# Performance work log

Measured on AMD Instinct MI355X. Metric: run time of the kernel, lower is better.

## Reference

```python
import jax, jax.numpy as jnp
import numpy as np

B, H, W, C = 2, 256, 256, 96
HEADS, WS, K = 6, 16, 64
HID = C // 8          # MoE hidden (reduction=8)
MLP = 2 * C           # mlp_ratio=2
KS = 5                # convffn / lepe kernel
N = H * W
WSQ = WS * WS
HEAD_D = C // HEADS


def _dwconv(x, w, b, pad):
    # x: [B,C,H,W], w: [C,1,k,k] depthwise conv
    y = jax.lax.conv_general_dilated(x, w, (1, 1), [(pad, pad), (pad, pad)],
        dimension_numbers=('NCHW', 'OIHW', 'NCHW'), feature_group_count=x.shape[1])
    return y + b[None, :, None, None]


def _ln(x, g, b):
    mu = x.mean(-1, keepdims=True)
    var = ((x - mu) ** 2).mean(-1, keepdims=True)
    return (x - mu) * jax.lax.rsqrt(var + 1e-5) * g + b


def _gelu(x):
    return jax.nn.gelu(x, approximate=False)


def _lrelu(x):
    return jnp.where(x >= 0, x, 0.2 * x)


def _make_rpi():
    coords = np.stack(np.meshgrid(np.arange(WS), np.arange(WS), indexing='ij'))
    cf = coords.reshape(2, -1)
    rel = (cf[:, :, None] - cf[:, None, :]).transpose(1, 2, 0).astype(np.int32)
    rel[..., 0] += WS - 1
    rel[..., 1] += WS - 1
    rel[..., 0] *= 2 * WS - 1
    return jnp.asarray(rel.sum(-1))  # [WSQ, WSQ]


def setup_inputs():
    key = jax.random.key(0)
    ks = iter(jax.random.split(key, 64))
    nrm = lambda shape, s=0.02: jax.random.normal(next(ks), shape, jnp.float32) * s
    inp = {}
    inp['x'] = jax.random.normal(next(ks), (B, N, C), jnp.float32)
    inp['n1_g'] = jnp.ones((C,), jnp.float32); inp['n1_b'] = jnp.zeros((C,), jnp.float32)
    inp['n2_g'] = jnp.ones((C,), jnp.float32); inp['n2_b'] = jnp.zeros((C,), jnp.float32)
    inp['g_w1'] = nrm((HID, C)); inp['g_b1'] = jnp.zeros((HID,), jnp.float32)
    inp['g_w2'] = nrm((3, HID)); inp['g_b2'] = jnp.zeros((3,), jnp.float32)
    for i, k_sz in zip((1, 2, 3), (3, 5, 7)):
        inp[f'e{i}_w1'] = nrm((HID, C)); inp[f'e{i}_b1'] = jnp.zeros((HID,), jnp.float32)
        inp[f'e{i}_pw'] = nrm((HID, HID))
        inp[f'e{i}_dw'] = nrm((HID, 1, k_sz, k_sz), 0.1); inp[f'e{i}_dwb'] = jnp.zeros((HID,), jnp.float32)
        inp[f'e{i}_w2'] = nrm((C, HID)); inp[f'e{i}_b2'] = jnp.zeros((C,), jnp.float32)
    inp['moe_scale'] = jnp.full((1,), 0.001, jnp.float32)
    inp['qkv_w'] = nrm((3 * C, C)); inp['qkv_b'] = jnp.zeros((3 * C,), jnp.float32)
    inp['lepe_w'] = nrm((C, 1, KS, KS), 0.1); inp['lepe_b'] = jnp.zeros((C,), jnp.float32)
    inp['rpb'] = nrm(((2 * WS - 1) ** 2, HEADS))
    inp['proj_w'] = nrm((C, C)); inp['proj_b'] = jnp.zeros((C,), jnp.float32)
    inp['fc1_w'] = nrm((MLP, C)); inp['fc1_b'] = jnp.zeros((MLP,), jnp.float32)
    inp['ffn_dw'] = nrm((MLP, 1, KS, KS), 0.1); inp['ffn_db'] = jnp.zeros((MLP,), jnp.float32)
    inp['fc2_w'] = nrm((C, MLP)); inp['fc2_b'] = jnp.zeros((C,), jnp.float32)
    inp['rpi'] = _make_rpi()
    return inp


def _forward(x, n1_g, n1_b, n2_g, n2_b, g_w1, g_b1, g_w2, g_b2,
             e1_w1, e1_b1, e1_pw, e1_dw, e1_dwb, e1_w2, e1_b2,
             e2_w1, e2_b1, e2_pw, e2_dw, e2_dwb, e2_w2, e2_b2,
             e3_w1, e3_b1, e3_pw, e3_dw, e3_dwb, e3_w2, e3_b2,
             moe_scale, qkv_w, qkv_b, lepe_w, lepe_b, rpb, proj_w, proj_b,
             fc1_w, fc1_b, ffn_dw, ffn_db, fc2_w, fc2_b, rpi):
    b, n, c = x.shape
    shortcut = x
    y = _ln(x, n1_g, n1_b)
    img = y.reshape(b, H, W, c).transpose(0, 3, 1, 2)  # [b,c,H,W]

    # ---- MultiScaleMoEBlock ----
    pooled = img.mean((2, 3))                                   # [b,c]
    g = jax.nn.relu(pooled @ g_w1.T + g_b1)
    g = jax.nn.softmax(g @ g_w2.T + g_b2, axis=-1)              # [b,3]

    def expert(z, w1, b1, pw, dw, dwb, w2, b2, pad):
        t = _lrelu(jnp.einsum('bchw,oc->bohw', z, w1) + b1[None, :, None, None])
        t = jnp.einsum('bchw,oc->bohw', t, pw)                  # BSConvU pw (no bias)
        t = _lrelu(_dwconv(t, dw, dwb, pad))                    # BSConvU dw
        return jnp.einsum('bchw,oc->bohw', t, w2) + b2[None, :, None, None]

    o = (g[:, 0, None, None, None] * expert(img, e1_w1, e1_b1, e1_pw, e1_dw, e1_dwb, e1_w2, e1_b2, 1)
         + g[:, 1, None, None, None] * expert(img, e2_w1, e2_b1, e2_pw, e2_dw, e2_dwb, e2_w2, e2_b2, 2)
         + g[:, 2, None, None, None] * expert(img, e3_w1, e3_b1, e3_pw, e3_dw, e3_dwb, e3_w2, e3_b2, 3))
    img = img + o * moe_scale[0]
    y = img.transpose(0, 2, 3, 1).reshape(b, n, c)

    # ---- qkv + LePE ----
    qkv = y @ qkv_w.T + qkv_b                                   # [b,n,3c]
    v = qkv[..., 2 * c:]
    vimg = v.reshape(b, H, W, c).transpose(0, 3, 1, 2)
    lepe = _gelu(_dwconv(vimg, lepe_w, lepe_b, (KS - 1) // 2)).transpose(0, 2, 3, 1).reshape(b, n, c)
    xq = jnp.concatenate([qkv, lepe], -1).reshape(b, H, W, 4 * c)

    # ---- window partition (shift=0) ----
    win = xq.reshape(b, H // WS, WS, W // WS, WS, 4 * c).transpose(0, 1, 3, 2, 4, 5).reshape(-1, WSQ, 4 * c)
    Bw = win.shape[0]
    qkvl = win.reshape(Bw, WSQ, 4, HEADS, HEAD_D).transpose(2, 0, 3, 1, 4)
    q, k_, vv, lp = qkvl[0], qkvl[1], qkvl[2], qkvl[3]          # each [Bw,H,N,d]

    attn = jnp.einsum('bhnd,bhmd->bhnm', q * (HEAD_D ** -0.5), k_)
    bias = rpb[rpi].transpose(2, 0, 1)                          # [heads,WSQ,WSQ]
    attn = jax.nn.softmax(attn + bias[None], axis=-1)

    # top-k progressive focused attention (first layer: pfa is None)
    vals, idx = jax.lax.top_k(attn, K)                          # [Bw,heads,WSQ,K]
    bi = jnp.arange(Bw)[:, None, None, None]
    hi = jnp.arange(HEADS)[None, :, None, None]
    ni = jnp.arange(WSQ)[None, None, :, None]
    attn_s = jnp.zeros_like(attn).at[bi, hi, ni, idx].set(vals)
    out = jnp.einsum('bhnm,bhmd->bhnd', attn_s, vv) + lp
    out = out.transpose(0, 2, 1, 3).reshape(Bw, WSQ, c)
    out = out @ proj_w.T + proj_b

    # ---- window reverse ----
    out = out.reshape(b, H // WS, W // WS, WS, WS, c).transpose(0, 1, 3, 2, 4, 5).reshape(b, n, c)
    x = shortcut + out

    # ---- ConvFFN ----
    y = _ln(x, n2_g, n2_b)
    t = _gelu(y @ fc1_w.T + fc1_b)
    timg = t.reshape(b, H, W, MLP).transpose(0, 3, 1, 2)
    t = t + _gelu(_dwconv(timg, ffn_dw, ffn_db, (KS - 1) // 2)).transpose(0, 2, 3, 1).reshape(b, n, MLP)
    x = x + (t @ fc2_w.T + fc2_b)
    return x


def reference(x, n1_g, n1_b, n2_g, n2_b, g_w1, g_b1, g_w2, g_b2,
              e1_w1, e1_b1, e1_pw, e1_dw, e1_dwb, e1_w2, e1_b2,
              e2_w1, e2_b1, e2_pw, e2_dw, e2_dwb, e2_w2, e2_b2,
              e3_w1, e3_b1, e3_pw, e3_dw, e3_dwb, e3_w2, e3_b2,
              moe_scale, qkv_w, qkv_b, lepe_w, lepe_b, rpb, proj_w, proj_b,
              fc1_w, fc1_b, ffn_dw, ffn_db, fc2_w, fc2_b, rpi):
    return _forward(x, n1_g, n1_b, n2_g, n2_b, g_w1, g_b1, g_w2, g_b2,
                    e1_w1, e1_b1, e1_pw, e1_dw, e1_dwb, e1_w2, e1_b2,
                    e2_w1, e2_b1, e2_pw, e2_dw, e2_dwb, e2_w2, e2_b2,
                    e3_w1, e3_b1, e3_pw, e3_dw, e3_dwb, e3_w2, e3_b2,
                    moe_scale, qkv_w, qkv_b, lepe_w, lepe_b, rpb, proj_w, proj_b,
                    fc1_w, fc1_b, ffn_dw, ffn_db, fc2_w, fc2_b, rpi)
```

## Files before the change

### kernel.cpp

```cpp
#include <hip/hip_runtime.h>
#include <cstdint>

#define BB 2
#define HH_ 256
#define WW_ 256
#define CC 96
#define NTOK 65536
#define MTOK 131072
#define HEADS 6
#define WS 16
#define WSQ 256
#define HEAD_D 16
#define TOPK 64
#define HID 12
#define MLP_ 192

typedef short v8s __attribute__((ext_vector_type(8)));
typedef float v4f __attribute__((ext_vector_type(4)));

__device__ __forceinline__ float gelu_f(float v) {
  return 0.5f * v * (1.0f + erff(v * 0.70710678118654752440f));
}
__device__ __forceinline__ float lrelu_f(float v) { return v >= 0.0f ? v : 0.2f * v; }
__device__ __forceinline__ unsigned short bf16r(float f) {
  unsigned u = __float_as_uint(f);
  unsigned r = u + 0x7fffu + ((u >> 16) & 1u);
  return (unsigned short)(r >> 16);
}
__device__ __forceinline__ float bf16d(unsigned short h) {
  return __uint_as_float(((unsigned)h) << 16);
}

__global__ __launch_bounds__(256) void ln_kernel(const float* __restrict__ in,
    const float* __restrict__ gam, const float* __restrict__ bet, float* __restrict__ out) {
  int wid = blockIdx.x * 4 + (threadIdx.x >> 6);
  int lane = threadIdx.x & 63;
  const float* row = in + (size_t)wid * CC;
  float v0 = row[lane];
  float v1 = (lane < 32) ? row[64 + lane] : 0.0f;
  float s = v0 + v1;
  #pragma unroll
  for (int off = 32; off; off >>= 1) s += __shfl_xor(s, off);
  float mean = s * (1.0f / 96.0f);
  float d0 = v0 - mean;
  float d1 = (lane < 32) ? (v1 - mean) : 0.0f;
  float q = d0 * d0 + d1 * d1;
  #pragma unroll
  for (int off = 32; off; off >>= 1) q += __shfl_xor(q, off);
  float r = rsqrtf(q * (1.0f / 96.0f) + 1e-5f);
  float* orow = out + (size_t)wid * CC;
  orow[lane] = d0 * r * gam[lane] + bet[lane];
  if (lane < 32) orow[64 + lane] = d1 * r * gam[64 + lane] + bet[64 + lane];
}

__global__ __launch_bounds__(128) void pool_kernel(const float* __restrict__ A, float* __restrict__ pooled) {
  int c = threadIdx.x;
  if (c >= CC) return;
  int b = blockIdx.y;
  int t0 = blockIdx.x * 512;
  const float* base = A + ((size_t)b * NTOK + t0) * CC + c;
  float acc = 0.0f;
  #pragma unroll 8
  for (int t = 0; t < 512; t++) acc += base[(size_t)t * CC];
  atomicAdd(&pooled[b * CC + c], acc);
}

__global__ __launch_bounds__(64) void gate_kernel(const float* __restrict__ pooled,
    const float* __restrict__ w1, const float* __restrict__ b1,
    const float* __restrict__ w2, const float* __restrict__ b2, float* __restrict__ gv) {
  __shared__ float hb[BB][HID];
  __shared__ float lb[BB][3];
  int tid = threadIdx.x;
  if (tid < BB * HID) {
    int b = tid / HID, o = tid % HID;
    float s = b1[o];
    for (int c = 0; c < CC; c++) s += (pooled[b * CC + c] * (1.0f / 65536.0f)) * w1[o * CC + c];
    hb[b][o] = fmaxf(s, 0.0f);
  }
  __syncthreads();
  if (tid < BB * 3) {
    int b = tid / 3, j = tid % 3;
    float s = b2[j];
    for (int o = 0; o < HID; o++) s += hb[b][o] * w2[j * HID + o];
    lb[b][j] = s;
  }
  __syncthreads();
  if (tid < BB) {
    float m = fmaxf(lb[tid][0], fmaxf(lb[tid][1], lb[tid][2]));
    float e0 = __expf(lb[tid][0] - m), e1 = __expf(lb[tid][1] - m), e2 = __expf(lb[tid][2] - m);
    float inv = 1.0f / (e0 + e1 + e2);
    gv[tid * 3 + 0] = e0 * inv; gv[tid * 3 + 1] = e1 * inv; gv[tid * 3 + 2] = e2 * inv;
  }
}

template <int K, int NO, int ACT, bool RESID, bool HASB>
__global__ __launch_bounds__(256, 4) void mgemm_kernel(const float* __restrict__ A,
    const float* __restrict__ W, const float* __restrict__ bias,
    const float* __restrict__ resid, float* __restrict__ out, int ostride, int rstride) {
  __shared__ __align__(16) unsigned short al[128][104];
  __shared__ __align__(16) unsigned short wl[64][104];
  int tid = threadIdx.x;
  int lane = tid & 63, wv = tid >> 6, quad = lane >> 4, to = lane & 15;
  int o0 = blockIdx.x * 64, p0 = blockIdx.y * 128;
  v4f acc[2][4];
  #pragma unroll
  for (int ni = 0; ni < 4; ni++) {
    float bv = 0.0f;
    if (HASB) { int o = o0 + ni * 16 + to; if (o < NO) bv = bias[o]; }
    #pragma unroll
    for (int mi = 0; mi < 2; mi++) acc[mi][ni] = (v4f){bv, bv, bv, bv};
  }
  for (int kc = 0; kc < K; kc += 96) {
    __syncthreads();
    {
      int r = tid & 127, half = tid >> 7;
      const float* ap = A + (size_t)(p0 + r) * K + kc + half * 48;
      #pragma unroll
      for (int g = 0; g < 3; g++) {
        float4 f0 = *(const float4*)(ap + g * 16);
        float4 f1 = *(const float4*)(ap + g * 16 + 4);
        float4 f2 = *(const float4*)(ap + g * 16 + 8);
        float4 f3 = *(const float4*)(ap + g * 16 + 12);
        uint4 u, v;
        u.x = (unsigned)bf16r(f0.x) | ((unsigned)bf16r(f0.y) << 16);
        u.y = (unsigned)bf16r(f0.z) | ((unsigned)bf16r(f0.w) << 16);
        u.z = (unsigned)bf16r(f1.x) | ((unsigned)bf16r(f1.y) << 16);
        u.w = (unsigned)bf16r(f1.z) | ((unsigned)bf16r(f1.w) << 16);
        v.x = (unsigned)bf16r(f2.x) | ((unsigned)bf16r(f2.y) << 16);
        v.y = (unsigned)bf16r(f2.z) | ((unsigned)bf16r(f2.w) << 16);
        v.z = (unsigned)bf16r(f3.x) | ((unsigned)bf16r(f3.y) << 16);
        v.w = (unsigned)bf16r(f3.z) | ((unsigned)bf16r(f3.w) << 16);
        *(uint4*)&al[r][half * 48 + g * 16] = u;
        *(uint4*)&al[r][half * 48 + g * 16 + 8] = v;
      }
    }
    {
      int r = tid & 63, q = tid >> 6;
      int o = o0 + r;
      if (o < NO) {
        const float* wp = W + (size_t)o * K + kc + q * 24;
        #pragma unroll
        for (int g = 0; g < 3; g++) {
          float4 f0 = *(const float4*)(wp + g * 8);
          float4 f1 = *(const float4*)(wp + g * 8 + 4);
          uint4 u;
          u.x = (unsigned)bf16r(f0.x) | ((unsigned)bf16r(f0.y) << 16);
          u.y = (unsigned)bf16r(f0.z) | ((unsigned)bf16r(f0.w) << 16);
          u.z = (unsigned)bf16r(f1.x) | ((unsigned)bf16r(f1.y) << 16);
          u.w = (unsigned)bf16r(f1.z) | ((unsigned)bf16r(f1.w) << 16);
          *(uint4*)&wl[r][q * 24 + g * 8] = u;
        }
      } else {
        uint4 z = make_uint4(0, 0, 0, 0);
        #pragma unroll
        for (int g = 0; g < 3; g++) *(uint4*)&wl[r][q * 24 + g * 8] = z;
      }
    }
    __syncthreads();
    #pragma unroll
    for (int ks = 0; ks < 3; ks++) {
      v8s af[2], bfr[4];
      #pragma unroll
      for (int mi = 0; mi < 2; mi++)
        af[mi] = *(const v8s*)&al[wv * 32 + mi * 16 + to][ks * 32 + quad * 8];
      #pragma unroll
      for (int ni = 0; ni < 4; ni++)
        bfr[ni] = *(const v8s*)&wl[ni * 16 + to][ks * 32 + quad * 8];
      #pragma unroll
      for (int mi = 0; mi < 2; mi++)
        #pragma unroll
        for (int ni = 0; ni < 4; ni++)
          acc[mi][ni] = __builtin_amdgcn_mfma_f32_16x16x32_bf16(af[mi], bfr[ni], acc[mi][ni], 0, 0, 0);
    }
  }
  #pragma unroll
  for (int mi = 0; mi < 2; mi++)
    #pragma unroll
    for (int ni = 0; ni < 4; ni++) {
      int o = o0 + ni * 16 + to;
      if (o < NO) {
        #pragma unroll
        for (int rg = 0; rg < 4; rg++) {
          int p = p0 + wv * 32 + mi * 16 + quad * 4 + rg;
          float v = acc[mi][ni][rg];
          if (ACT == 1) v = lrelu_f(v);
          else if (ACT == 2) v = gelu_f(v);
          if (RESID) v += resid[(size_t)p * rstride + o];
          out[(size_t)p * ostride + o] = v;
        }
      }
    }
}

template <int K, int KC, int NO, int ACT, bool RESID, bool HASB>
__global__ __launch_bounds__(256) void gemm_kernel(const float* __restrict__ in,
    const float* __restrict__ w, const float* __restrict__ bias,
    const float* __restrict__ resid, float* __restrict__ out, int ostride, int rstride) {
  __shared__ __align__(16) float xs[64][KC + 4];
  __shared__ __align__(16) float ws[64][KC + 4];
  int tid = threadIdx.x;
  int p0 = blockIdx.x * 64;
  int o0 = blockIdx.y * 64;
  int to = tid & 15, tp = tid >> 4;
  float acc[4][4];
  #pragma unroll
  for (int j = 0; j < 4; j++) {
    float bv = 0.0f;
    if (HASB) { int o = o0 + to + 16 * j; if (o < NO) bv = bias[o]; }
    #pragma unroll
    for (int i = 0; i < 4; i++) acc[i][j] = bv;
  }
  for (int kc = 0; kc < K; kc += KC) {
    __syncthreads();
    for (int idx = tid; idx < 64 * (KC / 4); idx += 256) {
      int p = idx / (KC / 4), c4 = idx % (KC / 4);
      *(float4*)&xs[p][c4 * 4] = *(const float4*)&in[(size_t)(p0 + p) * K + kc + c4 * 4];
    }
    for (int idx = tid; idx < 64 * (KC / 4); idx += 256) {
      int r = idx / (KC / 4), c4 = idx % (KC / 4);
      int o = o0 + r;
      float4 v = make_float4(0.f, 0.f, 0.f, 0.f);
      if (o < NO) v = *(const float4*)&w[(size_t)o * K + kc + c4 * 4];
      *(float4*)&ws[r][c4 * 4] = v;
    }
    __syncthreads();
    #pragma unroll 4
    for (int cc = 0; cc < KC; cc += 4) {
      float4 xv[4], wv[4];
      #pragma unroll
      for (int i = 0; i < 4; i++) xv[i] = *(const float4*)&xs[tp + 16 * i][cc];
      #pragma unroll
      for (int j = 0; j < 4; j++) wv[j] = *(const float4*)&ws[to + 16 * j][cc];
      #pragma unroll
      for (int i = 0; i < 4; i++)
        #pragma unroll
        for (int j = 0; j < 4; j++)
          acc[i][j] += xv[i].x * wv[j].x + xv[i].y * wv[j].y + xv[i].z * wv[j].z + xv[i].w * wv[j].w;
    }
  }
  #pragma unroll
  for (int i = 0; i < 4; i++) {
    int p = p0 + tp + 16 * i;
    #pragma unroll
    for (int j = 0; j < 4; j++) {
      int o = o0 + to + 16 * j;
      if (o < NO) {
        float v = acc[i][j];
        if (ACT == 1) v = lrelu_f(v);
        else if (ACT == 2) v = gelu_f(v);
        if (RESID) v += resid[(size_t)p * rstride + o];
        out[(size_t)p * ostride + o] = v;
      }
    }
  }
}

template <int KSZ, int CH, int ACT, bool RESID>
__global__ __launch_bounds__(256) void dwconv_kernel(const float* __restrict__ in,
    const float* __restrict__ wt, const float* __restrict__ wb,
    const float* __restrict__ resid, float* __restrict__ out,
    int istride, int ostride, int rstride) {
  constexpr int C4 = CH / 4;
  constexpr int K2 = KSZ * KSZ;
  int e = blockIdx.x * 256 + threadIdx.x;
  int c4 = e % C4;
  int pix = e / C4;
  int b = pix >> 16, n = pix & 65535, h = n >> 8, w = n & 255;
  const int P = (KSZ - 1) / 2;
  int c = c4 * 4;
  float4 acc = *(const float4*)(wb + c);
  #pragma unroll
  for (int ky = 0; ky < KSZ; ky++) {
    int hh = h + ky - P;
    if (hh < 0 || hh >= HH_) continue;
    #pragma unroll
    for (int kx = 0; kx < KSZ; kx++) {
      int ww = w + kx - P;
      if (ww < 0 || ww >= WW_) continue;
      float4 iv = *(const float4*)(in + ((size_t)(b << 16) + (hh << 8) + ww) * istride + c);
      int t = ky * KSZ + kx;
      acc.x += wt[(c + 0) * K2 + t] * iv.x;
      acc.y += wt[(c + 1) * K2 + t] * iv.y;
      acc.z += wt[(c + 2) * K2 + t] * iv.z;
      acc.w += wt[(c + 3) * K2 + t] * iv.w;
    }
  }
  if (ACT == 1) {
    acc.x = lrelu_f(acc.x); acc.y = lrelu_f(acc.y); acc.z = lrelu_f(acc.z); acc.w = lrelu_f(acc.w);
  } else if (ACT == 2) {
    acc.x = gelu_f(acc.x); acc.y = gelu_f(acc.y); acc.z = gelu_f(acc.z); acc.w = gelu_f(acc.w);
  }
  if (RESID) {
    float4 rv = *(const float4*)(resid + (size_t)pix * rstride + c);
    acc.x += rv.x; acc.y += rv.y; acc.z += rv.z; acc.w += rv.w;
  }
  *(float4*)(out + (size_t)pix * ostride + c) = acc;
}

template <int KSZ, int CH, int ACT, bool RESID>
__global__ __launch_bounds__(256) void dwconv4_kernel(const float* __restrict__ in,
    const float* __restrict__ wt, const float* __restrict__ wb,
    const float* __restrict__ resid, float* __restrict__ out,
    int istride, int ostride, int rstride) {
  constexpr int C4 = CH / 4;
  constexpr int K2 = KSZ * KSZ;
  constexpr int P = (KSZ - 1) / 2;
  constexpr int NC = KSZ + 3;
  int e = blockIdx.x * 256 + threadIdx.x;
  int c4 = e % C4;
  int g = e / C4;
  int b = g >> 14, rem = g & 16383, h = rem >> 6, w0 = (rem & 63) << 2;
  int c = c4 * 4;
  float4 wbv = *(const float4*)(wb + c);
  float4 acc[4] = {wbv, wbv, wbv, wbv};
  #pragma unroll
  for (int ky = 0; ky < KSZ; ky++) {
    int hh = h + ky - P;
    if (hh < 0 || hh >= HH_) continue;
    const float* rowp = in + ((size_t)(b << 16) + (hh << 8)) * istride + c;
    float4 iv[NC];
    #pragma unroll
    for (int k = 0; k < NC; k++) {
      int ww = w0 - P + k;
      if (ww >= 0 && ww < WW_) iv[k] = *(const float4*)(rowp + (size_t)ww * istride);
      else iv[k] = make_float4(0.f, 0.f, 0.f, 0.f);
    }
    #pragma unroll
    for (int kx = 0; kx < KSZ; kx++) {
      int t = ky * KSZ + kx;
      float wt0 = wt[(c + 0) * K2 + t];
      float wt1 = wt[(c + 1) * K2 + t];
      float wt2 = wt[(c + 2) * K2 + t];
      float wt3 = wt[(c + 3) * K2 + t];
      #pragma unroll
      for (int px = 0; px < 4; px++) {
        acc[px].x += wt0 * iv[kx + px].x;
        acc[px].y += wt1 * iv[kx + px].y;
        acc[px].z += wt2 * iv[kx + px].z;
        acc[px].w += wt3 * iv[kx + px].w;
      }
    }
  }
  #pragma unroll
  for (int px = 0; px < 4; px++) {
    float4 a = acc[px];
    if (ACT == 1) {
      a.x = lrelu_f(a.x); a.y = lrelu_f(a.y); a.z = lrelu_f(a.z); a.w = lrelu_f(a.w);
    } else if (ACT == 2) {
      a.x = gelu_f(a.x); a.y = gelu_f(a.y); a.z = gelu_f(a.z); a.w = gelu_f(a.w);
    }
    size_t pix = (size_t)(b << 16) + (h << 8) + w0 + px;
    if (RESID) {
      float4 rv = *(const float4*)(resid + pix * rstride + c);
      a.x += rv.x; a.y += rv.y; a.z += rv.z; a.w += rv.w;
    }
    *(float4*)(out + pix * ostride + c) = a;
  }
}

__global__ __launch_bounds__(256) void moe_combine_kernel(float* __restrict__ A,
    const float* __restrict__ t3a, const float* __restrict__ t3b, const float* __restrict__ t3c,
    const float* __restrict__ w2a, const float* __restrict__ w2b, const float* __restrict__ w2c,
    const float* __restrict__ b2a, const float* __restrict__ b2b, const float* __restrict__ b2c,
    const float* __restrict__ gv, const float* __restrict__ ms) {
  int e4 = blockIdx.x * 256 + threadIdx.x;
  int c4 = e4 % (CC / 4), pix = e4 / (CC / 4), b = pix >> 16;
  int c = c4 * 4;
  float4 sa = *(const float4*)(b2a + c);
  float4 sb = *(const float4*)(b2b + c);
  float4 sc = *(const float4*)(b2c + c);
  #pragma unroll
  for (int h2 = 0; h2 < HID; h2++) {
    float ta = t3a[(size_t)pix * HID + h2];
    float tb = t3b[(size_t)pix * HID + h2];
    float tc = t3c[(size_t)pix * HID + h2];
    sa.x += ta * w2a[(c + 0) * HID + h2]; sa.y += ta * w2a[(c + 1) * HID + h2];
    sa.z += ta * w2a[(c + 2) * HID + h2]; sa.w += ta * w2a[(c + 3) * HID + h2];
    sb.x += tb * w2b[(c + 0) * HID + h2]; sb.y += tb * w2b[(c + 1) * HID + h2];
    sb.z += tb * w2b[(c + 2) * HID + h2]; sb.w += tb * w2b[(c + 3) * HID + h2];
    sc.x += tc * w2c[(c + 0) * HID + h2]; sc.y += tc * w2c[(c + 1) * HID + h2];
    sc.z += tc * w2c[(c + 2) * HID + h2]; sc.w += tc * w2c[(c + 3) * HID + h2];
  }
  float g0 = gv[b * 3 + 0], g1 = gv[b * 3 + 1], g2 = gv[b * 3 + 2], m0 = ms[0];
  float* ap = A + (size_t)pix * CC + c;
  float4 av = *(const float4*)ap;
  av.x += m0 * (g0 * sa.x + g1 * sb.x + g2 * sc.x);
  av.y += m0 * (g0 * sa.y + g1 * sb.y + g2 * sc.y);
  av.z += m0 * (g0 * sa.z + g1 * sb.z + g2 * sc.z);
  av.w += m0 * (g0 * sa.w + g1 * sb.w + g2 * sc.w);
  *(float4*)ap = av;
}

__global__ __launch_bounds__(256) void bias_kernel(const int* __restrict__ rpi,
    const float* __restrict__ rpb, float* __restrict__ biasT) {
  int idx = blockIdx.x * 256 + threadIdx.x;
  int h = idx >> 16, nm = idx & 65535;
  int n = nm >> 8, m = nm & 255;
  biasT[(h << 16) + ((n >> 2) << 10) + (m << 2) + (n & 3)] = rpb[rpi[nm] * HEADS + h];
}

__global__ __launch_bounds__(256, 3) void attn_kernel(const float* __restrict__ X,
    const float* __restrict__ biasT, float* __restrict__ O) {
  __shared__ __align__(16) unsigned short kb[256][16];
  __shared__ __align__(16) unsigned short vt[16][264];
  __shared__ __align__(16) unsigned short sS[4][16][264];
  int tid = threadIdx.x;
  int wi = blockIdx.x, hh = blockIdx.y;
  int b = wi >> 8, wrem = wi & 255, wy = wrem >> 4, wx = wrem & 15;
  int lane = tid & 63, wv_ = tid >> 6, quad = lane >> 4, to = lane & 15;

  {
    int m = tid;
    int nm = (((wy << 4) + (m >> 4)) << 8) | ((wx << 4) + (m & 15));
    size_t xb = ((size_t)(b << 16) + nm) * 288 + hh * 16;
    float kr[16], vr[16];
    *(float4*)&kr[0]  = *(const float4*)(X + xb + 96);
    *(float4*)&kr[4]  = *(const float4*)(X + xb + 100);
    *(float4*)&kr[8]  = *(const float4*)(X + xb + 104);
    *(float4*)&kr[12] = *(const float4*)(X + xb + 108);
    *(float4*)&vr[0]  = *(const float4*)(X + xb + 192);
    *(float4*)&vr[4]  = *(const float4*)(X + xb + 196);
    *(float4*)&vr[8]  = *(const float4*)(X + xb + 200);
    *(float4*)&vr[12] = *(const float4*)(X + xb + 204);
    unsigned u_[8];
    #pragma unroll
    for (int i = 0; i < 8; i++)
      u_[i] = (unsigned)bf16r(kr[2 * i]) | ((unsigned)bf16r(kr[2 * i + 1]) << 16);
    *(uint4*)&kb[m][0] = make_uint4(u_[0], u_[1], u_[2], u_[3]);
    *(uint4*)&kb[m][8] = make_uint4(u_[4], u_[5], u_[6], u_[7]);
    #pragma unroll
    for (int d = 0; d < 16; d++) vt[d][m] = bf16r(vr[d]);
  }

  auto load_q = [&](int ch) -> v8s {
    v8s af = {0, 0, 0, 0, 0, 0, 0, 0};
    if (quad < 2) {
      int nq = (((wy << 4) + ch) << 8) | ((wx << 4) + to);
      const float* qp = X + ((size_t)(b << 16) + nq) * 288 + hh * 16 + quad * 8;
      float4 f0 = *(const float4*)qp;
      float4 f1 = *(const float4*)(qp + 4);
      uint4 u;
      u.x = (unsigned)bf16r(f0.x * 0.25f) | ((unsigned)bf16r(f0.y * 0.25f) << 16);
      u.y = (unsigned)bf16r(f0.z * 0.25f) | ((unsigned)bf16r(f0.w * 0.25f) << 16);
      u.z = (unsigned)bf16r(f1.x * 0.25f) | ((unsigned)bf16r(f1.y * 0.25f) << 16);
      u.w = (unsigned)bf16r(f1.z * 0.25f) | ((unsigned)bf16r(f1.w * 0.25f) << 16);
      af = *(v8s*)&u;
    }
    return af;
  };

  v8s afc = load_q(wv_ * 4);
  __syncthreads();

  unsigned short (*sw)[264] = sS[wv_];

  #pragma unroll 1
  for (int j = 0; j < 4; j++) {
    int ch = wv_ * 4 + j;
    int r0 = ch * 16;
    int n_o = (((wy << 4) + ch) << 8) | ((wx << 4) + (quad << 2));
    size_t ob = ((size_t)(b << 16) + n_o) * CC + hh * 16 + to;
    float oc0 = O[ob], oc1 = O[ob + 96], oc2 = O[ob + 192], oc3 = O[ob + 288];
    #pragma unroll
    for (int t = 0; t < 16; t++) {
      v8s bfr = {0, 0, 0, 0, 0, 0, 0, 0};
      if (quad < 2) bfr = *(const v8s*)&kb[t * 16 + to][quad * 8];
      float4 bv = *(const float4*)(biasT + ((size_t)hh << 16) +
                                   (size_t)(((r0 >> 2) + quad) << 10) + ((t * 16 + to) << 2));
      v4f cf;
      cf[0] = bv.x; cf[1] = bv.y; cf[2] = bv.z; cf[3] = bv.w;
      cf = __builtin_amdgcn_mfma_f32_16x16x32_bf16(afc, bfr, cf, 0, 0, 0);
      #pragma unroll
      for (int rg = 0; rg < 4; rg++)
        sw[quad * 4 + rg][t * 16 + to] = (unsigned short)(__float_as_uint(cf[rg]) >> 16);
    }
    if (j < 3) afc = load_q(ch + 1);
    #pragma unroll 1
    for (int g = 0; g < 4; g++) {
      float ex_[4][4], inv_[4];
      unsigned uk[4][4], cand[4];
      int hb[4]; bool done[4];
      #pragma unroll
      for (int qr = 0; qr < 4; qr++) {
        int r = g * 4 + qr;
        unsigned h0 = sw[r][lane], h1 = sw[r][64 + lane];
        unsigned h2 = sw[r][128 + lane], h3 = sw[r][192 + lane];
        float x0 = __uint_as_float(h0 << 16), x1 = __uint_as_float(h1 << 16);
        float x2 = __uint_as_float(h2 << 16), x3 = __uint_as_float(h3 << 16);
        float mx = fmaxf(fmaxf(x0, x1), fmaxf(x2, x3));
        #pragma unroll
        for (int off = 32; off; off >>= 1) mx = fmaxf(mx, __shfl_xor(mx, off));
        float e0 = __expf(x0 - mx), e1 = __expf(x1 - mx), e2 = __expf(x2 - mx), e3 = __expf(x3 - mx);
        float sm = e0 + e1 + e2 + e3;
        #pragma unroll
        for (int off = 32; off; off >>= 1) sm += __shfl_xor(sm, off);
        inv_[qr] = 1.0f / sm;
        ex_[qr][0] = e0; ex_[qr][1] = e1; ex_[qr][2] = e2; ex_[qr][3] = e3;
        unsigned u0 = (h0 & 0x8000u) ? (h0 ^ 0xFFFFu) : (h0 | 0x8000u);
        unsigned u1 = (h1 & 0x8000u) ? (h1 ^ 0xFFFFu) : (h1 | 0x8000u);
        unsigned u2 = (h2 & 0x8000u) ? (h2 ^ 0xFFFFu) : (h2 | 0x8000u);
        unsigned u3 = (h3 & 0x8000u) ? (h3 ^ 0xFFFFu) : (h3 | 0x8000u);
        uk[qr][0] = u0; uk[qr][1] = u1; uk[qr][2] = u2; uk[qr][3] = u3;
        unsigned ad = u0 & u1 & u2 & u3;
        unsigned orr = u0 | u1 | u2 | u3;
        #pragma unroll
        for (int off = 32; off; off >>= 1) {
          ad &= __shfl_xor(ad, off);
          orr |= __shfl_xor(orr, off);
        }
        unsigned diff = ad ^ orr;
        hb[qr] = diff ? (31 - __builtin_clz(diff)) : -1;
        unsigned lowmask = (hb[qr] < 0) ? 0u : ((1u << (hb[qr] + 1)) - 1u);
        cand[qr] = ad & ~lowmask;
        done[qr] = (hb[qr] < 0);
      }
      int hbmax = max(max(hb[0], hb[1]), max(hb[2], hb[3]));
      for (int bit = hbmax; bit >= 0; --bit) {
        if (done[0] && done[1] && done[2] && done[3]) break;
        #pragma unroll
        for (int qr = 0; qr < 4; qr++) {
          if (done[qr] || bit > hb[qr]) continue;
          unsigned t = cand[qr] | (1u << bit);
          int cnt = __popcll(__ballot(uk[qr][0] >= t)) + __popcll(__ballot(uk[qr][1] >= t)) +
                    __popcll(__ballot(uk[qr][2] >= t)) + __popcll(__ballot(uk[qr][3] >= t));
          if (cnt >= TOPK) { cand[qr] = t; if (cnt == TOPK) done[qr] = true; }
        }
      }
      #pragma unroll
      for (int qr = 0; qr < 4; qr++) {
        int r = g * 4 + qr;
        unsigned c_ = cand[qr];
        int gcnt = __popcll(__ballot(uk[qr][0] > c_)) + __popcll(__ballot(uk[qr][1] > c_)) +
                   __popcll(__ballot(uk[qr][2] > c_)) + __popcll(__ballot(uk[qr][3] > c_));
        int need = TOPK - gcnt;
        unsigned long long q0 = __ballot(uk[qr][0] == c_), q1 = __ballot(uk[qr][1] == c_);
        unsigned long long q2 = __ballot(uk[qr][2] == c_), q3 = __ballot(uk[qr][3] == c_);
        unsigned long long lt = ((unsigned long long)1 << lane) - 1ull;
        int p0c = __popcll(q0 & lt);
        int p1c = __popcll(q0) + __popcll(q1 & lt);
        int p2c = __popcll(q0) + __popcll(q1) + __popcll(q2 & lt);
        int p3c = __popcll(q0) + __popcll(q1) + __popcll(q2) + __popcll(q3 & lt);
        float iv = inv_[qr];
        sw[r][lane]       = (uk[qr][0] > c_ || (uk[qr][0] == c_ && p0c < need)) ? bf16r(ex_[qr][0] * iv) : (unsigned short)0;
        sw[r][64 + lane]  = (uk[qr][1] > c_ || (uk[qr][1] == c_ && p1c < need)) ? bf16r(ex_[qr][1] * iv) : (unsigned short)0;
        sw[r][128 + lane] = (uk[qr][2] > c_ || (uk[qr][2] == c_ && p2c < need)) ? bf16r(ex_[qr][2] * iv) : (unsigned short)0;
        sw[r][192 + lane] = (uk[qr][3] > c_ || (uk[qr][3] == c_ && p3c < need)) ? bf16r(ex_[qr][3] * iv) : (unsigned short)0;
      }
    }
    v4f acc = {0.f, 0.f, 0.f, 0.f};
    #pragma unroll
    for (int kc = 0; kc < 8; kc++) {
      v8s paf = *(const v8s*)&sw[to][kc * 32 + quad * 8];
      v8s vbf = *(const v8s*)&vt[to][kc * 32 + quad * 8];
      acc = __builtin_amdgcn_mfma_f32_16x16x32_bf16(paf, vbf, acc, 0, 0, 0);
    }
    O[ob]       = oc0 + acc[0];
    O[ob + 96]  = oc1 + acc[1];
    O[ob + 192] = oc2 + acc[2];
    O[ob + 288] = oc3 + acc[3];
  }
}

extern "C" void kernel_launch(void* const* d_in, const int* in_sizes, int n_in,
                              void* d_out, int out_size, void* d_ws, size_t ws_size,
                              hipStream_t stream) {
  (void)in_sizes; (void)n_in; (void)out_size; (void)ws_size;
  const float* x     = (const float*)d_in[0];
  const float* n1_g  = (const float*)d_in[1];
  const float* n1_b  = (const float*)d_in[2];
  const float* n2_g  = (const float*)d_in[3];
  const float* n2_b  = (const float*)d_in[4];
  const float* g_w1  = (const float*)d_in[5];
  const float* g_b1  = (const float*)d_in[6];
  const float* g_w2  = (const float*)d_in[7];
  const float* g_b2  = (const float*)d_in[8];
  const float* e_w1[3]  = {(const float*)d_in[9],  (const float*)d_in[16], (const float*)d_in[23]};
  const float* e_b1[3]  = {(const float*)d_in[10], (const float*)d_in[17], (const float*)d_in[24]};
  const float* e_pw[3]  = {(const float*)d_in[11], (const float*)d_in[18], (const float*)d_in[25]};
  const float* e_dw[3]  = {(const float*)d_in[12], (const float*)d_in[19], (const float*)d_in[26]};
  const float* e_dwb[3] = {(const float*)d_in[13], (const float*)d_in[20], (const float*)d_in[27]};
  const float* e_w2[3]  = {(const float*)d_in[14], (const float*)d_in[21], (const float*)d_in[28]};
  const float* e_b2[3]  = {(const float*)d_in[15], (const float*)d_in[22], (const float*)d_in[29]};
  const float* ms    = (const float*)d_in[30];
  const float* qkv_w = (const float*)d_in[31];
  const float* qkv_b = (const float*)d_in[32];
  const float* lepe_w = (const float*)d_in[33];
  const float* lepe_b = (const float*)d_in[34];
  const float* rpb   = (const float*)d_in[35];
  const float* proj_w = (const float*)d_in[36];
  const float* proj_b = (const float*)d_in[37];
  const float* fc1_w = (const float*)d_in[38];
  const float* fc1_b = (const float*)d_in[39];
  const float* ffn_dw = (const float*)d_in[40];
  const float* ffn_db = (const float*)d_in[41];
  const float* fc2_w = (const float*)d_in[42];
  const float* fc2_b = (const float*)d_in[43];
  const int*   rpi   = (const int*)d_in[44];
  float* out = (float*)d_out;

  const size_t M = MTOK;
  float* ws = (float*)d_ws;
  float* A   = ws;
  float* t1  = ws + 96 * M;
  float* t2b = ws + 108 * M;
  float* t3[3] = { ws + 120 * M, ws + 132 * M, ws + 144 * M };
  float* X   = ws + 96 * M;
  float* T   = ws + 192 * M;
  float* T2  = ws;
  float* O   = A;
  float* S2  = out;
  float* biasT = out;
  float* pooled = ws + 384 * M;
  float* gv = pooled + 192;

  bias_kernel<<<HEADS * NTOK / 256, 256, 0, stream>>>(rpi, rpb, biasT);
  ln_kernel<<<M / 4, 256, 0, stream>>>(x, n1_g, n1_b, A);
  hipMemsetAsync(pooled, 0, 256 * sizeof(float), stream);
  pool_kernel<<<dim3(128, 2), 128, 0, stream>>>(A, pooled);
  gate_kernel<<<1, 64, 0, stream>>>(pooled, g_w1, g_b1, g_w2, g_b2, gv);
  for (int i = 0; i < 3; i++) {
    mgemm_kernel<96, 12, 1, false, true><<<dim3(1, 1024), 256, 0, stream>>>(
        A, e_w1[i], e_b1[i], nullptr, t1, 12, 0);
    gemm_kernel<12, 12, 12, 0, false, false><<<dim3(2048, 1), 256, 0, stream>>>(
        t1, e_pw[i], nullptr, nullptr, t2b, 12, 0);
    if (i == 0)
      dwconv_kernel<3, 12, 1, false><<<M * 3 / 256, 256, 0, stream>>>(t2b, e_dw[0], e_dwb[0], nullptr, t3[0], 12, 12, 0);
    else if (i == 1)
      dwconv_kernel<5, 12, 1, false><<<M * 3 / 256, 256, 0, stream>>>(t2b, e_dw[1], e_dwb[1], nullptr, t3[1], 12, 12, 0);
    else
      dwconv_kernel<7, 12, 1, false><<<M * 3 / 256, 256, 0, stream>>>(t2b, e_dw[2], e_dwb[2], nullptr, t3[2], 12, 12, 0);
  }
  moe_combine_kernel<<<M * 24 / 256, 256, 0, stream>>>(A,
      t3[0], t3[1], t3[2], e_w2[0], e_w2[1], e_w2[2], e_b2[0], e_b2[1], e_b2[2], gv, ms);
  mgemm_kernel<96, 288, 0, false, true><<<dim3(5, 1024), 256, 0, stream>>>(
      A, qkv_w, qkv_b, nullptr, X, 288, 0);
  dwconv4_kernel<5, 96, 2, false><<<M * 6 / 256, 256, 0, stream>>>(X + 192, lepe_w, lepe_b, nullptr, O, 288, 96, 0);
  attn_kernel<<<dim3(512, 6), 256, 0, stream>>>(X, biasT, O);
  mgemm_kernel<96, 96, 0, true, true><<<dim3(2, 1024), 256, 0, stream>>>(
      O, proj_w, proj_b, x, S2, 96, 96);
  ln_kernel<<<M / 4, 256, 0, stream>>>(S2, n2_g, n2_b, A);
  mgemm_kernel<96, 192, 2, false, true><<<dim3(3, 1024), 256, 0, stream>>>(
      A, fc1_w, fc1_b, nullptr, T, 192, 0);
  dwconv4_kernel<5, 192, 2, true><<<M * 12 / 256, 256, 0, stream>>>(T, ffn_dw, ffn_db, T, T2, 192, 192, 192);
  mgemm_kernel<192, 96, 0, true, true><<<dim3(2, 1024), 256, 0, stream>>>(
      T2, fc2_w, fc2_b, S2, out, 96, 96);
}
```

Before: 1.792 ms.

## Hold V fragments in registers and swizzle score LDS to raise attention occupancy

The V transpose is staged through the per-wave score buffers, then each lane loads its eight V MFMA fragments into registers, so the separate vt LDS array is no longer needed. The score buffers drop their padding and use an XOR swizzle on the column index to avoid bank conflicts. With less LDS per block, the launch bound goes from 3 to 4 blocks per CU. In exchange there is an extra __syncthreads, 32 more VGPRs per lane for V, and a risk of register spills at the tighter bound.

Measured after the change: 1.920 ms. 7.1% more time.

```diff
diff --git a/kernel.cpp b/kernel.cpp
--- a/kernel.cpp
+++ b/kernel.cpp
@@ -399,15 +399,17 @@
   biasT[(h << 16) + ((n >> 2) << 10) + (m << 2) + (n & 3)] = rpb[rpi[nm] * HEADS + h];
 }
 
-__global__ __launch_bounds__(256, 3) void attn_kernel(const float* __restrict__ X,
+__device__ __forceinline__ int swz(int r, int c) { return r * 256 + (c ^ (r << 3)); }
+
+__global__ __launch_bounds__(256, 4) void attn_kernel(const float* __restrict__ X,
     const float* __restrict__ biasT, float* __restrict__ O) {
   __shared__ __align__(16) unsigned short kb[256][16];
-  __shared__ __align__(16) unsigned short vt[16][264];
-  __shared__ __align__(16) unsigned short sS[4][16][264];
+  __shared__ __align__(16) unsigned short sS[4][4096];
   int tid = threadIdx.x;
   int wi = blockIdx.x, hh = blockIdx.y;
   int b = wi >> 8, wrem = wi & 255, wy = wrem >> 4, wx = wrem & 15;
   int lane = tid & 63, wv_ = tid >> 6, quad = lane >> 4, to = lane & 15;
+  unsigned short* sw = &sS[wv_][0];
 
   {
     int m = tid;
@@ -429,7 +431,7 @@
     *(uint4*)&kb[m][0] = make_uint4(u_[0], u_[1], u_[2], u_[3]);
     *(uint4*)&kb[m][8] = make_uint4(u_[4], u_[5], u_[6], u_[7]);
     #pragma unroll
-    for (int d = 0; d < 16; d++) vt[d][m] = bf16r(vr[d]);
+    for (int d = 0; d < 16; d++) sw[d * 64 + lane] = bf16r(vr[d]);
   }
 
   auto load_q = [&](int ch) -> v8s {
@@ -452,7 +454,11 @@
   v8s afc = load_q(wv_ * 4);
   __syncthreads();
 
-  unsigned short (*sw)[264] = sS[wv_];
+  v8s vreg[8];
+  #pragma unroll
+  for (int kc = 0; kc < 8; kc++)
+    vreg[kc] = *(const v8s*)&sS[kc >> 1][to * 64 + (kc & 1) * 32 + quad * 8];
+  __syncthreads();
 
   #pragma unroll 1
   for (int j = 0; j < 4; j++) {
@@ -472,7 +478,7 @@
       cf = __builtin_amdgcn_mfma_f32_16x16x32_bf16(afc, bfr, cf, 0, 0, 0);
       #pragma unroll
       for (int rg = 0; rg < 4; rg++)
-        sw[quad * 4 + rg][t * 16 + to] = (unsigned short)(__float_as_uint(cf[rg]) >> 16);
+        sw[swz(quad * 4 + rg, t * 16 + to)] = (unsigned short)(__float_as_uint(cf[rg]) >> 16);
     }
     if (j < 3) afc = load_q(ch + 1);
     #pragma unroll 1
@@ -483,8 +489,8 @@
       #pragma unroll
       for (int qr = 0; qr < 4; qr++) {
         int r = g * 4 + qr;
-        unsigned h0 = sw[r][lane], h1 = sw[r][64 + lane];
-        unsigned h2 = sw[r][128 + lane], h3 = sw[r][192 + lane];
+        unsigned h0 = sw[swz(r, lane)], h1 = sw[swz(r, 64 + lane)];
+        unsigned h2 = sw[swz(r, 128 + lane)], h3 = sw[swz(r, 192 + lane)];
         float x0 = __uint_as_float(h0 << 16), x1 = __uint_as_float(h1 << 16);
         float x2 = __uint_as_float(h2 << 16), x3 = __uint_as_float(h3 << 16);
         float mx = fmaxf(fmaxf(x0, x1), fmaxf(x2, x3));
@@ -541,18 +547,17 @@
         int p2c = __popcll(q0) + __popcll(q1) + __popcll(q2 & lt);
         int p3c = __popcll(q0) + __popcll(q1) + __popcll(q2) + __popcll(q3 & lt);
         float iv = inv_[qr];
-        sw[r][lane]       = (uk[qr][0] > c_ || (uk[qr][0] == c_ && p0c < need)) ? bf16r(ex_[qr][0] * iv) : (unsigned short)0;
-        sw[r][64 + lane]  = (uk[qr][1] > c_ || (uk[qr][1] == c_ && p1c < need)) ? bf16r(ex_[qr][1] * iv) : (unsigned short)0;
-        sw[r][128 + lane] = (uk[qr][2] > c_ || (uk[qr][2] == c_ && p2c < need)) ? bf16r(ex_[qr][2] * iv) : (unsigned short)0;
-        sw[r][192 + lane] = (uk[qr][3] > c_ || (uk[qr][3] == c_ && p3c < need)) ? bf16r(ex_[qr][3] * iv) : (unsigned short)0;
+        sw[swz(r, lane)]       = (uk[qr][0] > c_ || (uk[qr][0] == c_ && p0c < need)) ? bf16r(ex_[qr][0] * iv) : (unsigned short)0;
+        sw[swz(r, 64 + lane)]  = (uk[qr][1] > c_ || (uk[qr][1] == c_ && p1c < need)) ? bf16r(ex_[qr][1] * iv) : (unsigned short)0;
+        sw[swz(r, 128 + lane)] = (uk[qr][2] > c_ || (uk[qr][2] == c_ && p2c < need)) ? bf16r(ex_[qr][2] * iv) : (unsigned short)0;
+        sw[swz(r, 192 + lane)] = (uk[qr][3] > c_ || (uk[qr][3] == c_ && p3c < need)) ? bf16r(ex_[qr][3] * iv) : (unsigned short)0;
       }
     }
     v4f acc = {0.f, 0.f, 0.f, 0.f};
     #pragma unroll
     for (int kc = 0; kc < 8; kc++) {
-      v8s paf = *(const v8s*)&sw[to][kc * 32 + quad * 8];
-      v8s vbf = *(const v8s*)&vt[to][kc * 32 + quad * 8];
-      acc = __builtin_amdgcn_mfma_f32_16x16x32_bf16(paf, vbf, acc, 0, 0, 0);
+      v8s paf = *(const v8s*)&sw[swz(to, kc * 32 + quad * 8)];
+      acc = __builtin_amdgcn_mfma_f32_16x16x32_bf16(paf, vreg[kc], acc, 0, 0, 0);
     }
     O[ob]       = oc0 + acc[0];
     O[ob + 96]  = oc1 + acc[1];
```

## Split attention row chunks cooperatively across waves with double-buffered score tile

Applied to the files above, without the earlier changes.

Each 16-row query chunk of the window is now handled by all four waves together instead of one wave per chunk. Each wave computes a quarter of the score columns and then does softmax and top-k on four rows, while one rotating wave does the PV MFMA. The score scratch in shared memory shrinks from four per-wave tiles to two double-buffered tiles, which should allow more blocks per CU and spread the serial top-k work. The cost is two block-wide barriers per chunk (32 in total) and PV work done by only one wave at a time.

New measurement: 1.705 ms. -4.9%, faster.

```diff
diff --git a/kernel.cpp b/kernel.cpp
--- a/kernel.cpp
+++ b/kernel.cpp
@@ -403,7 +403,7 @@
     const float* __restrict__ biasT, float* __restrict__ O) {
   __shared__ __align__(16) unsigned short kb[256][16];
   __shared__ __align__(16) unsigned short vt[16][264];
-  __shared__ __align__(16) unsigned short sS[4][16][264];
+  __shared__ __align__(16) unsigned short sSb[2][16][264];
   int tid = threadIdx.x;
   int wi = blockIdx.x, hh = blockIdx.y;
   int b = wi >> 8, wrem = wi & 255, wy = wrem >> 4, wx = wrem & 15;
@@ -449,40 +449,44 @@
     return af;
   };
 
-  v8s afc = load_q(wv_ * 4);
+  v8s afc = load_q(0);
   __syncthreads();
 
-  unsigned short (*sw)[264] = sS[wv_];
-
   #pragma unroll 1
-  for (int j = 0; j < 4; j++) {
-    int ch = wv_ * 4 + j;
-    int r0 = ch * 16;
-    int n_o = (((wy << 4) + ch) << 8) | ((wx << 4) + (quad << 2));
-    size_t ob = ((size_t)(b << 16) + n_o) * CC + hh * 16 + to;
-    float oc0 = O[ob], oc1 = O[ob + 96], oc2 = O[ob + 192], oc3 = O[ob + 288];
-    #pragma unroll
-    for (int t = 0; t < 16; t++) {
+  for (int i = 0; i < 16; i++) {
+    unsigned short (*sw)[264] = sSb[i & 1];
+    int r0 = i * 16;
+    bool avw = (wv_ == (i & 3));
+    size_t ob = 0;
+    float oc0 = 0.f, oc1 = 0.f, oc2 = 0.f, oc3 = 0.f;
+    if (avw) {
+      int n_o = (((wy << 4) + i) << 8) | ((wx << 4) + (quad << 2));
+      ob = ((size_t)(b << 16) + n_o) * CC + hh * 16 + to;
+      oc0 = O[ob]; oc1 = O[ob + 96]; oc2 = O[ob + 192]; oc3 = O[ob + 288];
+    }
+    #pragma unroll
+    for (int t = 0; t < 4; t++) {
+      int c0 = (wv_ * 4 + t) * 16;
       v8s bfr = {0, 0, 0, 0, 0, 0, 0, 0};
-      if (quad < 2) bfr = *(const v8s*)&kb[t * 16 + to][quad * 8];
+      if (quad < 2) bfr = *(const v8s*)&kb[c0 + to][quad * 8];
       float4 bv = *(const float4*)(biasT + ((size_t)hh << 16) +
-                                   (size_t)(((r0 >> 2) + quad) << 10) + ((t * 16 + to) << 2));
+                                   (size_t)(((r0 >> 2) + quad) << 10) + ((c0 + to) << 2));
       v4f cf;
       cf[0] = bv.x; cf[1] = bv.y; cf[2] = bv.z; cf[3] = bv.w;
       cf = __builtin_amdgcn_mfma_f32_16x16x32_bf16(afc, bfr, cf, 0, 0, 0);
       #pragma unroll
       for (int rg = 0; rg < 4; rg++)
-        sw[quad * 4 + rg][t * 16 + to] = (unsigned short)(__float_as_uint(cf[rg]) >> 16);
-    }
-    if (j < 3) afc = load_q(ch + 1);
-    #pragma unroll 1
-    for (int g = 0; g < 4; g++) {
+        sw[quad * 4 + rg][c0 + to] = (unsigned short)(__float_as_uint(cf[rg]) >> 16);
+    }
+    if (i < 15) afc = load_q(i + 1);
+    __syncthreads();
+    {
       float ex_[4][4], inv_[4];
       unsigned uk[4][4], cand[4];
       int hb[4]; bool done[4];
       #pragma unroll
       for (int qr = 0; qr < 4; qr++) {
-        int r = g * 4 + qr;
+        int r = wv_ * 4 + qr;
         unsigned h0 = sw[r][lane], h1 = sw[r][64 + lane];
         unsigned h2 = sw[r][128 + lane], h3 = sw[r][192 + lane];
         float x0 = __uint_as_float(h0 << 16), x1 = __uint_as_float(h1 << 16);
@@ -528,7 +532,7 @@
       }
       #pragma unroll
       for (int qr = 0; qr < 4; qr++) {
-        int r = g * 4 + qr;
+        int r = wv_ * 4 + qr;
         unsigned c_ = cand[qr];
         int gcnt = __popcll(__ballot(uk[qr][0] > c_)) + __popcll(__ballot(uk[qr][1] > c_)) +
                    __popcll(__ballot(uk[qr][2] > c_)) + __popcll(__ballot(uk[qr][3] > c_));
@@ -547,17 +551,20 @@
         sw[r][192 + lane] = (uk[qr][3] > c_ || (uk[qr][3] == c_ && p3c < need)) ? bf16r(ex_[qr][3] * iv) : (unsigned short)0;
       }
     }
-    v4f acc = {0.f, 0.f, 0.f, 0.f};
-    #pragma unroll
-    for (int kc = 0; kc < 8; kc++) {
-      v8s paf = *(const v8s*)&sw[to][kc * 32 + quad * 8];
-      v8s vbf = *(const v8s*)&vt[to][kc * 32 + quad * 8];
-      acc = __builtin_amdgcn_mfma_f32_16x16x32_bf16(paf, vbf, acc, 0, 0, 0);
-    }
-    O[ob]       = oc0 + acc[0];
-    O[ob + 96]  = oc1 + acc[1];
-    O[ob + 192] = oc2 + acc[2];
-    O[ob + 288] = oc3 + acc[3];
+    __syncthreads();
+    if (avw) {
+      v4f acc = {0.f, 0.f, 0.f, 0.f};
+      #pragma unroll
+      for (int kc = 0; kc < 8; kc++) {
+        v8s paf = *(const v8s*)&sw[to][kc * 32 + quad * 8];
+        v8s vbf = *(const v8s*)&vt[to][kc * 32 + quad * 8];
+        acc = __builtin_amdgcn_mfma_f32_16x16x32_bf16(paf, vbf, acc, 0, 0, 0);
+      }
+      O[ob]       = oc0 + acc[0];
+      O[ob + 96]  = oc1 + acc[1];
+      O[ob + 192] = oc2 + acc[2];
+      O[ob + 288] = oc3 + acc[3];
+    }
   }
 }
 
```
